# Performance work log

Hardware: AMD Instinct MI355X
Metric: run time of the kernel (lower is better)

## Reference

```python
import jax, jax.numpy as jnp
import numpy as np

B, D, N = 8, 512, 4096
K = 2048  # codebook_size


def setup_inputs() -> dict:
    key = jax.random.key(0)
    k1, k2 = jax.random.split(key)
    x = jax.random.normal(k1, (B, D, N), dtype=jnp.float32)
    embed = jax.random.normal(k2, (K, D), dtype=jnp.float32)
    return {"x": x, "embed": embed}


def reference(x, embed):
    # x: [b, d, n] -> [b, n, d] (project_in is Identity since codebook_dim == dim)
    xt = jnp.transpose(x, (0, 2, 1))  # [b, n, d]
    # squared euclidean distances (argmin-equivalent to torch.cdist argmin)
    x2 = jnp.sum(xt * xt, axis=-1, keepdims=True)          # [b, n, 1]
    e2 = jnp.sum(embed * embed, axis=-1)                   # [k]
    cross = jnp.einsum("bnd,kd->bnk", xt, embed)           # [b, n, k]
    dist = x2 - 2.0 * cross + e2                           # [b, n, k]
    embed_ind = jnp.argmin(dist, axis=-1)                  # [b, n] int
    quantize = embed[embed_ind]                            # [b, n, d] gather
    # project_out Identity, then rearrange 'b n d -> b d n'
    quantize = jnp.transpose(quantize, (0, 2, 1))          # [b, d, n]
    return quantize, embed_ind
```

## Files before the change

### kernel.cpp

```cpp
#include <hip/hip_runtime.h>
#include <math.h>

#define DDIM 512
#define NNN  4096
#define KKK  2048
#define MMM  32768

#define TMQ  128
#define TNC  256
#define BK   32
#define KSPLIT 2
#define KHALF (KKK/KSPLIT)
#define NKT  (KHALF/TNC)
#define NDR  (DDIM/BK)
#define TOTR (NKT*NDR)
#define BUFS ((TMQ+TNC)*BK)
#define NBUF 3
#define TAU  0.05f
#define CAPF 4096

#define XH_OFF   0
#define EH_OFF   8388608
#define PART_OFF (EH_OFF + 524288)
#define XF_OFF   (PART_OFF + MMM*KSPLIT*4)
#define KEY_OFF  (XF_OFF + 2097152)
#define LIST_OFF (KEY_OFF + 8192)
#define CNT_OFF  (LIST_OFF + CAPF)
#define IDX_OFF  ((size_t)MMM * DDIM)

typedef short short8v __attribute__((ext_vector_type(8)));
typedef _Float16 half8v __attribute__((ext_vector_type(8)));
typedef float f32x4   __attribute__((ext_vector_type(4)));

__device__ inline unsigned short f2h(float f) {
  _Float16 h = (_Float16)f;
  return *(unsigned short*)&h;
}

__device__ inline void gl_lds16(const short* g, short* l) {
  __builtin_amdgcn_global_load_lds(
      (const __attribute__((address_space(1))) unsigned int*)g,
      (__attribute__((address_space(3))) unsigned int*)l, 16, 0, 0);
}

__device__ inline unsigned mono(float f) {
  unsigned u = __float_as_uint(f);
  return (u & 0x80000000u) ? ~u : (u | 0x80000000u);
}

__global__ __launch_bounds__(256)
void conv_xe(const float* __restrict__ x, const float* __restrict__ embed,
             float* __restrict__ halfe2, float* __restrict__ out) {
  __shared__ float xt[64][65];
  const int t = threadIdx.x;

  if (blockIdx.x >= 4096) {
    const int blk = blockIdx.x - 4096;
    const int gid = blk * 256 + t;
    if (gid == 0) *(int*)&out[CNT_OFF] = 0;
    if (gid < CAPF) ((unsigned long long*)&out[KEY_OFF])[gid] = ~0ull;
    const int row  = blk * 4 + (t >> 6);
    const int lane = t & 63;
    const float* e = embed + (size_t)row * DDIM;
    short* eh = (short*)&out[EH_OFF];
    const float4 v0 = *(const float4*)&e[lane*8];
    const float4 v1 = *(const float4*)&e[lane*8 + 4];
    const float vv[8] = {v0.x,v0.y,v0.z,v0.w,v1.x,v1.y,v1.z,v1.w};
    float s = 0.f;
    short8v p;
    #pragma unroll
    for (int i = 0; i < 8; ++i) { s = fmaf(vv[i], vv[i], s); p[i] = (short)f2h(vv[i]); }
    *(short8v*)&eh[(size_t)row * DDIM + lane*8] = p;
    #pragma unroll
    for (int off = 32; off >= 1; off >>= 1) s += __shfl_xor(s, off, 64);
    if (lane == 0) halfe2[row] = 0.5f * s;
    return;
  }

  const int nt = blockIdx.x & 63, dt = (blockIdx.x >> 6) & 7, b = blockIdx.x >> 9;
  const int n0 = nt * 64, d0 = dt * 64;
  const float* xb = x + ((size_t)b * DDIM + d0) * NNN + n0;
  #pragma unroll
  for (int i = 0; i < 4; ++i) {
    const int fid = t + 256*i;
    const int dl = fid >> 4, n4 = (fid & 15) * 4;
    const float4 v = *(const float4*)&xb[(size_t)dl * NNN + n4];
    xt[dl][n4+0] = v.x; xt[dl][n4+1] = v.y; xt[dl][n4+2] = v.z; xt[dl][n4+3] = v.w;
  }
  __syncthreads();
  short* xh = (short*)&out[XH_OFF];
  const int m0 = b * NNN + n0;
  #pragma unroll
  for (int i = 0; i < 2; ++i) {
    const int id = t + 256*i;
    const int m = id >> 3, ch = (id & 7) * 8;
    short8v p;
    #pragma unroll
    for (int j = 0; j < 8; ++j) p[j] = (short)f2h(xt[ch + j][m]);
    *(short8v*)&xh[(size_t)(m0 + m) * DDIM + d0 + ch] = p;
  }
}

__global__ __launch_bounds__(256, 2)
void vq_main(const float* __restrict__ halfe2, float* __restrict__ out) {
  __shared__ __align__(16) short lds[NBUF * BUFS];
  const short* xh = (const short*)&out[XH_OFF];
  const short* eh = (const short*)&out[EH_OFF];

  const int t  = threadIdx.x;
  const int mb = blockIdx.x >> 1, ks = blockIdx.x & 1;
  const int q0 = mb * TMQ;
  const int kbase = ks * KHALF;
  const int w = t >> 6, lane = t & 63;
  const int mw = (w >> 1) * 64, nw = (w & 1) * 128;
  const int l15 = lane & 15, lg = lane >> 4;
  const int c0 = w * 6;
  const int lrow = lane >> 2;
  const int scol = ((((lane & 3) - ((lane >> 3) & 3)) & 3) << 3);

  float rv1[16], rv2[16]; int ri1[16];
  #pragma unroll
  for (int i = 0; i < 16; ++i) { rv1[i] = INFINITY; rv2[i] = INFINITY; ri1[i] = 0x7FFFFFFF; }

  auto STAGE = [&](int R, int tb) {
    const int kt_ = R >> 4, dr_ = R & 15;
    const int kb_ = kbase + kt_ * TNC;
    const int d0_ = dr_ * BK;
    short* buf = lds + tb * BUFS;
    #pragma unroll
    for (int j = 0; j < 6; ++j) {
      const int c = c0 + j;
      const short* src = (c < 8)
        ? xh + (size_t)(q0 + c*16 + lrow) * DDIM + d0_ + scol
        : eh + (size_t)(kb_ + (c-8)*16 + lrow) * DDIM + d0_ + scol;
      gl_lds16(src, buf + c * 512);
    }
  };

  STAGE(0, 0);
  STAGE(1, 1);
  asm volatile("s_waitcnt vmcnt(6)" ::: "memory");
  __builtin_amdgcn_s_barrier();

  int bi = 0;
  for (int kt = 0; kt < NKT; ++kt) {
    const int kb = kbase + kt * TNC;
    f32x4 acc[4][8];
    #pragma unroll
    for (int mi = 0; mi < 4; ++mi)
      #pragma unroll
      for (int ni = 0; ni < 8; ++ni) acc[mi][ni] = (f32x4){0.f,0.f,0.f,0.f};

    for (int dr = 0; dr < NDR; ++dr) {
      const int R = kt * NDR + dr;
      const int nb = bi ? bi - 1 : 2;
      if (R + 2 < TOTR) STAGE(R + 2, nb);
      const short* xs = lds + bi * BUFS;
      const short* es = xs + TMQ * BK;
      half8v bfr[8];
      #pragma unroll
      for (int ni = 0; ni < 8; ++ni) {
        const int row = nw + ni*16 + l15;
        bfr[ni] = *(const half8v*)&es[row*32 + (((lg + (row >> 1)) & 3) << 3)];
      }
      #pragma unroll
      for (int mi = 0; mi < 4; ++mi) {
        const int row = mw + mi*16 + l15;
        const half8v a = *(const half8v*)&xs[row*32 + (((lg + (row >> 1)) & 3) << 3)];
        #pragma unroll
        for (int ni = 0; ni < 8; ++ni)
          acc[mi][ni] = __builtin_amdgcn_mfma_f32_16x16x32_f16(a, bfr[ni], acc[mi][ni], 0,0,0);
      }
      if (R + 2 < TOTR) { asm volatile("s_waitcnt vmcnt(6)" ::: "memory"); }
      else              { asm volatile("s_waitcnt vmcnt(0)" ::: "memory"); }
      __builtin_amdgcn_s_barrier();
      bi = (bi == 2) ? 0 : bi + 1;
    }

    float he[8];
    #pragma unroll
    for (int ni = 0; ni < 8; ++ni) he[ni] = halfe2[kb + nw + ni*16 + l15];
    #pragma unroll
    for (int mi = 0; mi < 4; ++mi) {
      #pragma unroll
      for (int r = 0; r < 4; ++r) {
        const int e_ = mi*4 + r;
        #pragma unroll
        for (int ni = 0; ni < 8; ++ni) {
          const float sc = he[ni] - acc[mi][ni][r];
          if (sc < rv1[e_]) { rv2[e_] = rv1[e_]; rv1[e_] = sc; ri1[e_] = kb + nw + ni*16 + l15; }
          else rv2[e_] = fminf(rv2[e_], sc);
        }
      }
    }
  }

  #pragma unroll
  for (int e_ = 0; e_ < 16; ++e_) {
    float v1 = rv1[e_], v2 = rv2[e_]; int i1 = ri1[e_];
    #pragma unroll
    for (int off = 1; off < 16; off <<= 1) {
      const float ov1 = __shfl_xor(v1, off, 64);
      const int   oi1 = __shfl_xor(i1, off, 64);
      const float ov2 = __shfl_xor(v2, off, 64);
      if (ov1 < v1 || (ov1 == v1 && oi1 < i1)) { v2 = fminf(v1, ov2); v1 = ov1; i1 = oi1; }
      else v2 = fminf(v2, ov1);
    }
    rv1[e_] = v1; rv2[e_] = v2; ri1[e_] = i1;
  }

  __syncthreads();
  float* mbuf = (float*)lds;
  if (l15 == 0) {
    #pragma unroll
    for (int mi = 0; mi < 4; ++mi)
      #pragma unroll
      for (int r = 0; r < 4; ++r) {
        const int ql = mw + mi*16 + lg*4 + r;
        const int slot = (ql*2 + (w & 1))*3;
        const int e_ = mi*4 + r;
        mbuf[slot+0] = rv1[e_];
        mbuf[slot+1] = __int_as_float(ri1[e_]);
        mbuf[slot+2] = rv2[e_];
      }
  }
  __syncthreads();
  if (t < TMQ) {
    const float a1 = mbuf[t*6+0]; const int ai = __float_as_int(mbuf[t*6+1]); const float a2 = mbuf[t*6+2];
    const float b1 = mbuf[t*6+3]; const int bi2 = __float_as_int(mbuf[t*6+4]); const float b2 = mbuf[t*6+5];
    float v1, v2; int i1;
    if (b1 < a1 || (b1 == a1 && bi2 < ai)) { v1 = b1; i1 = bi2; v2 = fminf(a1, b2); }
    else                                   { v1 = a1; i1 = ai;  v2 = fminf(a2, b1); }
    f32x4 st = {v1, (float)i1, v2, 0.f};
    *(f32x4*)&out[PART_OFF + ((size_t)(q0 + t)*KSPLIT + ks)*4] = st;
  }
}

__global__ void vq_merge(const float* __restrict__ x, float* __restrict__ out) {
  const int q = blockIdx.x * 256 + threadIdx.x;
  float v1, v2; int i1;
  {
    const f32x4 p = *(const f32x4*)&out[PART_OFF + (size_t)q*(KSPLIT*4)];
    v1 = p[0]; i1 = (int)p[1]; v2 = p[2];
  }
  #pragma unroll
  for (int s = 1; s < KSPLIT; ++s) {
    const f32x4 p = *(const f32x4*)&out[PART_OFF + (size_t)q*(KSPLIT*4) + s*4];
    const float b1 = p[0]; const int bi = (int)p[1]; const float b2 = p[2];
    if (b1 < v1 || (b1 == v1 && bi < i1)) { v2 = fminf(v1, b2); v1 = b1; i1 = bi; }
    else v2 = fminf(v2, b1);
  }
  out[IDX_OFF + q] = (float)i1;
  int pos = -1;
  if (v2 - v1 < TAU) {
    pos = atomicAdd((int*)&out[CNT_OFF], 1);
    if (pos < CAPF) ((int*)&out[LIST_OFF])[pos] = q;
    else pos = -1;
  }
  unsigned long long mask = __ballot(pos >= 0);
  const int lane = threadIdx.x & 63;
  float* XF = &out[XF_OFF];
  while (mask) {
    const int src = __ffsll(mask) - 1;
    mask &= mask - 1;
    const int qq = __shfl(q,   src, 64);
    const int pp = __shfl(pos, src, 64);
    const int bb = qq >> 12, nn = qq & (NNN - 1);
    const float* xb = x + (size_t)bb * DDIM * NNN + nn;
    #pragma unroll
    for (int j = 0; j < 8; ++j) {
      const int d = lane + 64*j;
      XF[(size_t)pp * DDIM + d] = xb[(size_t)d * NNN];
    }
  }
}

__global__ __launch_bounds__(256, 2)
void vq_refine(const float* __restrict__ embed, const float* __restrict__ halfe2,
               float* __restrict__ out) {
  const int nf0 = *(const int*)&out[CNT_OFF];
  const int nf  = nf0 < CAPF ? nf0 : CAPF;
  const int s0  = blockIdx.y * 64;
  if (s0 >= nf) return;
  __shared__ float xs[32][68];
  __shared__ float es[32][132];
  const int t = threadIdx.x, tx = t & 15, ty = t >> 4;
  const int kb = blockIdx.x * 128;
  const float* XF = &out[XF_OFF];
  unsigned long long* keys = (unsigned long long*)&out[KEY_OFF];

  float acc[4][8];
  #pragma unroll
  for (int i = 0; i < 4; ++i)
    #pragma unroll
    for (int j = 0; j < 8; ++j) acc[i][j] = 0.f;

  for (int dc = 0; dc < 16; ++dc) {
    __syncthreads();
    #pragma unroll
    for (int i = 0; i < 2; ++i) {
      const int l = t + 256*i;
      const int m = l >> 3, f = l & 7;
      const float4 v = *(const float4*)&XF[(size_t)(s0 + m) * DDIM + dc*32 + 4*f];
      xs[4*f+0][m] = v.x; xs[4*f+1][m] = v.y; xs[4*f+2][m] = v.z; xs[4*f+3][m] = v.w;
    }
    #pragma unroll
    for (int i = 0; i < 4; ++i) {
      const int l = t + 256*i;
      const int k = l >> 3, f = l & 7;
      const float4 v = *(const float4*)&embed[(size_t)(kb + k)*DDIM + dc*32 + 4*f];
      es[4*f+0][k] = v.x; es[4*f+1][k] = v.y; es[4*f+2][k] = v.z; es[4*f+3][k] = v.w;
    }
    __syncthreads();
    #pragma unroll
    for (int d = 0; d < 32; ++d) {
      const float4 a4 = *(const float4*)&xs[d][ty*4];
      const float4 b0 = *(const float4*)&es[d][tx*4];
      const float4 b1 = *(const float4*)&es[d][64 + tx*4];
      const float a[4]  = {a4.x, a4.y, a4.z, a4.w};
      const float bb[8] = {b0.x, b0.y, b0.z, b0.w, b1.x, b1.y, b1.z, b1.w};
      #pragma unroll
      for (int i = 0; i < 4; ++i)
        #pragma unroll
        for (int j = 0; j < 8; ++j)
          acc[i][j] = fmaf(a[i], bb[j], acc[i][j]);
    }
  }

  const int kb0 = kb + tx*4, kb1 = kb + 64 + tx*4;
  const float4 h0 = *(const float4*)&halfe2[kb0];
  const float4 h1 = *(const float4*)&halfe2[kb1];
  const float hh[8] = {h0.x, h0.y, h0.z, h0.w, h1.x, h1.y, h1.z, h1.w};
  #pragma unroll
  for (int i = 0; i < 4; ++i) {
    float v = hh[0] - acc[i][0];
    int  vi = kb0;
    #pragma unroll
    for (int j = 1; j < 8; ++j) {
      const float w  = hh[j] - acc[i][j];
      const int   wk = (j < 4) ? (kb0 + j) : (kb1 + j - 4);
      if (w < v) { v = w; vi = wk; }
    }
    #pragma unroll
    for (int off = 1; off < 16; off <<= 1) {
      const float ov = __shfl_xor(v, off, 64);
      const int   oi = __shfl_xor(vi, off, 64);
      if (ov < v || (ov == v && oi < vi)) { v = ov; vi = oi; }
    }
    if (tx == 0) {
      const unsigned long long key =
          ((unsigned long long)mono(v) << 32) | (unsigned)vi;
      atomicMin(&keys[s0 + ty*4 + i], key);
    }
  }
}

__global__ void vq_apply(float* __restrict__ out) {
  const int slot = blockIdx.x * 256 + threadIdx.x;
  const int nf0 = *(const int*)&out[CNT_OFF];
  const int nf  = nf0 < CAPF ? nf0 : CAPF;
  if (slot >= nf) return;
  const int q = ((const int*)&out[LIST_OFF])[slot];
  const unsigned long long k = ((const unsigned long long*)&out[KEY_OFF])[slot];
  if (k != ~0ull) out[IDX_OFF + q] = (float)(unsigned)(k & 0xFFFFFFFFull);
}

__global__ __launch_bounds__(256)
void vq_gather(const float* __restrict__ embed, float* __restrict__ out) {
  __shared__ float ls[32][516];
  __shared__ int idx_s[32];
  const int t  = threadIdx.x;
  const int q0 = blockIdx.x * 32;
  const int b  = q0 >> 12, n0 = q0 & (NNN-1);
  if (t < 32) idx_s[t] = (int)out[IDX_OFF + q0 + t];
  __syncthreads();
  {
    const int rh  = t >> 7;
    const int col = (t & 127) * 4;
    #pragma unroll
    for (int p = 0; p < 16; ++p) {
      const int r = p*2 + rh;
      const float4 v = *(const float4*)&embed[(size_t)idx_s[r]*DDIM + col];
      *(float4*)&ls[r][col] = v;
    }
  }
  __syncthreads();
  float* qb = out + (size_t)b * DDIM * NNN + n0;
  #pragma unroll
  for (int j = 0; j < 16; ++j) {
    const int d  = 32*j + (t >> 3);
    const int n4 = (t & 7) * 4;
    float4 v;
    v.x = ls[n4+0][d]; v.y = ls[n4+1][d]; v.z = ls[n4+2][d]; v.w = ls[n4+3][d];
    *(float4*)&qb[(size_t)d * NNN + n4] = v;
  }
}

extern "C" void kernel_launch(void* const* d_in, const int* in_sizes, int n_in,
                              void* d_out, int out_size, void* d_ws, size_t ws_size,
                              hipStream_t stream) {
  const float* x     = (const float*)d_in[0];
  const float* embed = (const float*)d_in[1];
  float* out    = (float*)d_out;
  float* halfe2 = (float*)d_ws;

  hipLaunchKernelGGL(conv_xe, dim3(4096 + KKK/4), dim3(256), 0, stream, x, embed, halfe2, out);
  hipLaunchKernelGGL(vq_main,  dim3((MMM/TMQ)*KSPLIT), dim3(256), 0, stream, halfe2, out);
  hipLaunchKernelGGL(vq_merge, dim3(MMM/256), dim3(256), 0, stream, x, out);
  hipLaunchKernelGGL(vq_refine,dim3(16, CAPF/64), dim3(256), 0, stream, embed, halfe2, out);
  hipLaunchKernelGGL(vq_apply, dim3(CAPF/256),dim3(256), 0, stream, out);
  hipLaunchKernelGGL(vq_gather,dim3(MMM/32),  dim3(256), 0, stream, embed, out);
}
```

Baseline: 267.1 us.

## Fuse split-K merge into main and apply into refine via last-block tickets

Removes two kernel launches by having the last-arriving block of each split pair merge partial argmin results inside vq_main, and the last refine block apply refined indices. It also shrinks the LDS pipeline from triple to double buffering with a full vmcnt(0) wait each step. This cuts launch overhead and intermediate global round trips. The price is atomic tickets and a shallower prefetch pipeline that may expose more load latency in the main GEMM loop.

```diff
diff --git a/kernel.cpp b/kernel.cpp
--- a/kernel.cpp
+++ b/kernel.cpp
@@ -15,7 +15,7 @@
 #define NDR  (DDIM/BK)
 #define TOTR (NKT*NDR)
 #define BUFS ((TMQ+TNC)*BK)
-#define NBUF 3
+#define NBUF 2
 #define TAU  0.05f
 #define CAPF 4096
 
@@ -26,6 +26,7 @@
 #define KEY_OFF  (XF_OFF + 2097152)
 #define LIST_OFF (KEY_OFF + 8192)
 #define CNT_OFF  (LIST_OFF + CAPF)
+#define TICK_OFF (CNT_OFF + 1)
 #define IDX_OFF  ((size_t)MMM * DDIM)
 
 typedef short short8v __attribute__((ext_vector_type(8)));
@@ -58,6 +59,7 @@
     const int blk = blockIdx.x - 4096;
     const int gid = blk * 256 + t;
     if (gid == 0) *(int*)&out[CNT_OFF] = 0;
+    if (gid < 257) ((int*)&out[TICK_OFF])[gid] = 0;
     if (gid < CAPF) ((unsigned long long*)&out[KEY_OFF])[gid] = ~0ull;
     const int row  = blk * 4 + (t >> 6);
     const int lane = t & 63;
@@ -102,7 +104,8 @@
 }
 
 __global__ __launch_bounds__(256, 2)
-void vq_main(const float* __restrict__ halfe2, float* __restrict__ out) {
+void vq_main(const float* __restrict__ x, const float* __restrict__ halfe2,
+             float* __restrict__ out) {
   __shared__ __align__(16) short lds[NBUF * BUFS];
   const short* xh = (const short*)&out[XH_OFF];
   const short* eh = (const short*)&out[EH_OFF];
@@ -122,11 +125,11 @@
   #pragma unroll
   for (int i = 0; i < 16; ++i) { rv1[i] = INFINITY; rv2[i] = INFINITY; ri1[i] = 0x7FFFFFFF; }
 
-  auto STAGE = [&](int R, int tb) {
+  auto STAGE = [&](int R) {
     const int kt_ = R >> 4, dr_ = R & 15;
     const int kb_ = kbase + kt_ * TNC;
     const int d0_ = dr_ * BK;
-    short* buf = lds + tb * BUFS;
+    short* buf = lds + (R & 1) * BUFS;
     #pragma unroll
     for (int j = 0; j < 6; ++j) {
       const int c = c0 + j;
@@ -137,12 +140,10 @@
     }
   };
 
-  STAGE(0, 0);
-  STAGE(1, 1);
-  asm volatile("s_waitcnt vmcnt(6)" ::: "memory");
+  STAGE(0);
+  asm volatile("s_waitcnt vmcnt(0)" ::: "memory");
   __builtin_amdgcn_s_barrier();
 
-  int bi = 0;
   for (int kt = 0; kt < NKT; ++kt) {
     const int kb = kbase + kt * TNC;
     f32x4 acc[4][8];
@@ -151,12 +152,13 @@
       #pragma unroll
       for (int ni = 0; ni < 8; ++ni) acc[mi][ni] = (f32x4){0.f,0.f,0.f,0.f};
 
+    #pragma unroll 2
     for (int dr = 0; dr < NDR; ++dr) {
       const int R = kt * NDR + dr;
-      const int nb = bi ? bi - 1 : 2;
-      if (R + 2 < TOTR) STAGE(R + 2, nb);
-      const short* xs = lds + bi * BUFS;
-      const short* es = xs + TMQ * BK;
+      const short* cur = lds + (R & 1) * BUFS;
+      if (R + 1 < TOTR) STAGE(R + 1);
+      const short* xs = cur;
+      const short* es = cur + TMQ * BK;
       half8v bfr[8];
       #pragma unroll
       for (int ni = 0; ni < 8; ++ni) {
@@ -171,10 +173,8 @@
         for (int ni = 0; ni < 8; ++ni)
           acc[mi][ni] = __builtin_amdgcn_mfma_f32_16x16x32_f16(a, bfr[ni], acc[mi][ni], 0,0,0);
       }
-      if (R + 2 < TOTR) { asm volatile("s_waitcnt vmcnt(6)" ::: "memory"); }
-      else              { asm volatile("s_waitcnt vmcnt(0)" ::: "memory"); }
+      asm volatile("s_waitcnt vmcnt(0)" ::: "memory");
       __builtin_amdgcn_s_barrier();
-      bi = (bi == 2) ? 0 : bi + 1;
     }
 
     float he[8];
@@ -225,40 +225,52 @@
       }
   }
   __syncthreads();
+  unsigned long long* PART = (unsigned long long*)&out[PART_OFF];
   if (t < TMQ) {
     const float a1 = mbuf[t*6+0]; const int ai = __float_as_int(mbuf[t*6+1]); const float a2 = mbuf[t*6+2];
     const float b1 = mbuf[t*6+3]; const int bi2 = __float_as_int(mbuf[t*6+4]); const float b2 = mbuf[t*6+5];
     float v1, v2; int i1;
     if (b1 < a1 || (b1 == a1 && bi2 < ai)) { v1 = b1; i1 = bi2; v2 = fminf(a1, b2); }
     else                                   { v1 = a1; i1 = ai;  v2 = fminf(a2, b1); }
-    f32x4 st = {v1, (float)i1, v2, 0.f};
-    *(f32x4*)&out[PART_OFF + ((size_t)(q0 + t)*KSPLIT + ks)*4] = st;
-  }
-}
-
-__global__ void vq_merge(const float* __restrict__ x, float* __restrict__ out) {
-  const int q = blockIdx.x * 256 + threadIdx.x;
-  float v1, v2; int i1;
-  {
-    const f32x4 p = *(const f32x4*)&out[PART_OFF + (size_t)q*(KSPLIT*4)];
-    v1 = p[0]; i1 = (int)p[1]; v2 = p[2];
-  }
-  #pragma unroll
-  for (int s = 1; s < KSPLIT; ++s) {
-    const f32x4 p = *(const f32x4*)&out[PART_OFF + (size_t)q*(KSPLIT*4) + s*4];
-    const float b1 = p[0]; const int bi = (int)p[1]; const float b2 = p[2];
-    if (b1 < v1 || (b1 == v1 && bi < i1)) { v2 = fminf(v1, b2); v1 = b1; i1 = bi; }
-    else v2 = fminf(v2, b1);
-  }
-  out[IDX_OFF + q] = (float)i1;
+    const unsigned long long pa =
+        ((unsigned long long)__float_as_uint(v1) << 32) | (unsigned)i1;
+    const unsigned long long pb = (unsigned long long)__float_as_uint(v2);
+    __hip_atomic_store(&PART[(size_t)(q0 + t)*4 + ks*2 + 0], pa,
+                       __ATOMIC_RELEASE, __HIP_MEMORY_SCOPE_AGENT);
+    __hip_atomic_store(&PART[(size_t)(q0 + t)*4 + ks*2 + 1], pb,
+                       __ATOMIC_RELEASE, __HIP_MEMORY_SCOPE_AGENT);
+  }
+  __syncthreads();
+  __shared__ int who;
+  int* tick = (int*)&out[TICK_OFF];
+  if (t == 0)
+    who = __hip_atomic_fetch_add(&tick[mb], 1, __ATOMIC_ACQ_REL, __HIP_MEMORY_SCOPE_AGENT);
+  __syncthreads();
+  if (who != 1) return;
+
   int pos = -1;
-  if (v2 - v1 < TAU) {
-    pos = atomicAdd((int*)&out[CNT_OFF], 1);
-    if (pos < CAPF) ((int*)&out[LIST_OFF])[pos] = q;
-    else pos = -1;
+  const int q = q0 + (t & 127);
+  if (t < TMQ) {
+    const unsigned long long a0 = __hip_atomic_load(&PART[(size_t)q*4 + 0], __ATOMIC_ACQUIRE, __HIP_MEMORY_SCOPE_AGENT);
+    const unsigned long long a1 = __hip_atomic_load(&PART[(size_t)q*4 + 1], __ATOMIC_ACQUIRE, __HIP_MEMORY_SCOPE_AGENT);
+    const unsigned long long b0 = __hip_atomic_load(&PART[(size_t)q*4 + 2], __ATOMIC_ACQUIRE, __HIP_MEMORY_SCOPE_AGENT);
+    const unsigned long long b1 = __hip_atomic_load(&PART[(size_t)q*4 + 3], __ATOMIC_ACQUIRE, __HIP_MEMORY_SCOPE_AGENT);
+    float v1 = __uint_as_float((unsigned)(a0 >> 32));
+    int   i1 = (int)(unsigned)a0;
+    float v2 = __uint_as_float((unsigned)a1);
+    const float w1 = __uint_as_float((unsigned)(b0 >> 32));
+    const int   wi = (int)(unsigned)b0;
+    const float w2 = __uint_as_float((unsigned)b1);
+    if (w1 < v1 || (w1 == v1 && wi < i1)) { v2 = fminf(v1, w2); v1 = w1; i1 = wi; }
+    else v2 = fminf(v2, w1);
+    out[IDX_OFF + q] = (float)i1;
+    if (v2 - v1 < TAU) {
+      pos = atomicAdd((int*)&out[CNT_OFF], 1);
+      if (pos < CAPF) ((int*)&out[LIST_OFF])[pos] = q;
+      else pos = -1;
+    }
   }
   unsigned long long mask = __ballot(pos >= 0);
-  const int lane = threadIdx.x & 63;
   float* XF = &out[XF_OFF];
   while (mask) {
     const int src = __ffsll(mask) - 1;
@@ -281,7 +293,6 @@
   const int nf0 = *(const int*)&out[CNT_OFF];
   const int nf  = nf0 < CAPF ? nf0 : CAPF;
   const int s0  = blockIdx.y * 64;
-  if (s0 >= nf) return;
   __shared__ float xs[32][68];
   __shared__ float es[32][132];
   const int t = threadIdx.x, tx = t & 15, ty = t >> 4;
@@ -289,80 +300,87 @@
   const float* XF = &out[XF_OFF];
   unsigned long long* keys = (unsigned long long*)&out[KEY_OFF];
 
-  float acc[4][8];
-  #pragma unroll
-  for (int i = 0; i < 4; ++i)
-    #pragma unroll
-    for (int j = 0; j < 8; ++j) acc[i][j] = 0.f;
-
-  for (int dc = 0; dc < 16; ++dc) {
-    __syncthreads();
-    #pragma unroll
-    for (int i = 0; i < 2; ++i) {
-      const int l = t + 256*i;
-      const int m = l >> 3, f = l & 7;
-      const float4 v = *(const float4*)&XF[(size_t)(s0 + m) * DDIM + dc*32 + 4*f];
-      xs[4*f+0][m] = v.x; xs[4*f+1][m] = v.y; xs[4*f+2][m] = v.z; xs[4*f+3][m] = v.w;
-    }
+  if (s0 < nf) {
+    float acc[4][8];
+    #pragma unroll
+    for (int i = 0; i < 4; ++i)
+      #pragma unroll
+      for (int j = 0; j < 8; ++j) acc[i][j] = 0.f;
+
+    for (int dc = 0; dc < 16; ++dc) {
+      __syncthreads();
+      #pragma unroll
+      for (int i = 0; i < 2; ++i) {
+        const int l = t + 256*i;
+        const int m = l >> 3, f = l & 7;
+        const float4 v = *(const float4*)&XF[(size_t)(s0 + m) * DDIM + dc*32 + 4*f];
+        xs[4*f+0][m] = v.x; xs[4*f+1][m] = v.y; xs[4*f+2][m] = v.z; xs[4*f+3][m] = v.w;
+      }
+      #pragma unroll
+      for (int i = 0; i < 4; ++i) {
+        const int l = t + 256*i;
+        const int k = l >> 3, f = l & 7;
+        const float4 v = *(const float4*)&embed[(size_t)(kb + k)*DDIM + dc*32 + 4*f];
+        es[4*f+0][k] = v.x; es[4*f+1][k] = v.y; es[4*f+2][k] = v.z; es[4*f+3][k] = v.w;
+      }
+      __syncthreads();
+      #pragma unroll
+      for (int d = 0; d < 32; ++d) {
+        const float4 a4 = *(const float4*)&xs[d][ty*4];
+        const float4 b0 = *(const float4*)&es[d][tx*4];
+        const float4 b1 = *(const float4*)&es[d][64 + tx*4];
+        const float a[4]  = {a4.x, a4.y, a4.z, a4.w};
+        const float bb[8] = {b0.x, b0.y, b0.z, b0.w, b1.x, b1.y, b1.z, b1.w};
+        #pragma unroll
+        for (int i = 0; i < 4; ++i)
+          #pragma unroll
+          for (int j = 0; j < 8; ++j)
+            acc[i][j] = fmaf(a[i], bb[j], acc[i][j]);
+      }
+    }
+
+    const int kb0 = kb + tx*4, kb1 = kb + 64 + tx*4;
+    const float4 h0 = *(const float4*)&halfe2[kb0];
+    const float4 h1 = *(const float4*)&halfe2[kb1];
+    const float hh[8] = {h0.x, h0.y, h0.z, h0.w, h1.x, h1.y, h1.z, h1.w};
     #pragma unroll
     for (int i = 0; i < 4; ++i) {
-      const int l = t + 256*i;
-      const int k = l >> 3, f = l & 7;
-      const float4 v = *(const float4*)&embed[(size_t)(kb + k)*DDIM + dc*32 + 4*f];
-      es[4*f+0][k] = v.x; es[4*f+1][k] = v.y; es[4*f+2][k] = v.z; es[4*f+3][k] = v.w;
-    }
-    __syncthreads();
-    #pragma unroll
-    for (int d = 0; d < 32; ++d) {
-      const float4 a4 = *(const float4*)&xs[d][ty*4];
-      const float4 b0 = *(const float4*)&es[d][tx*4];
-      const float4 b1 = *(const float4*)&es[d][64 + tx*4];
-      const float a[4]  = {a4.x, a4.y, a4.z, a4.w};
-      const float bb[8] = {b0.x, b0.y, b0.z, b0.w, b1.x, b1.y, b1.z, b1.w};
-      #pragma unroll
-      for (int i = 0; i < 4; ++i)
-        #pragma unroll
-        for (int j = 0; j < 8; ++j)
-          acc[i][j] = fmaf(a[i], bb[j], acc[i][j]);
-    }
-  }
-
-  const int kb0 = kb + tx*4, kb1 = kb + 64 + tx*4;
-  const float4 h0 = *(const float4*)&halfe2[kb0];
-  const float4 h1 = *(const float4*)&halfe2[kb1];
-  const float hh[8] = {h0.x, h0.y, h0.z, h0.w, h1.x, h1.y, h1.z, h1.w};
-  #pragma unroll
-  for (int i = 0; i < 4; ++i) {
-    float v = hh[0] - acc[i][0];
-    int  vi = kb0;
-    #pragma unroll
-    for (int j = 1; j < 8; ++j) {
-      const float w  = hh[j] - acc[i][j];
-      const int   wk = (j < 4) ? (kb0 + j) : (kb1 + j - 4);
-      if (w < v) { v = w; vi = wk; }
-    }
-    #pragma unroll
-    for (int off = 1; off < 16; off <<= 1) {
-      const float ov = __shfl_xor(v, off, 64);
-      const int   oi = __shfl_xor(vi, off, 64);
-      if (ov < v || (ov == v && oi < vi)) { v = ov; vi = oi; }
-    }
-    if (tx == 0) {
-      const unsigned long long key =
-          ((unsigned long long)mono(v) << 32) | (unsigned)vi;
-      atomicMin(&keys[s0 + ty*4 + i], key);
-    }
-  }
-}
-
-__global__ void vq_apply(float* __restrict__ out) {
-  const int slot = blockIdx.x * 256 + threadIdx.x;
-  const int nf0 = *(const int*)&out[CNT_OFF];
-  const int nf  = nf0 < CAPF ? nf0 : CAPF;
-  if (slot >= nf) return;
-  const int q = ((const int*)&out[LIST_OFF])[slot];
-  const unsigned long long k = ((const unsigned long long*)&out[KEY_OFF])[slot];
-  if (k != ~0ull) out[IDX_OFF + q] = (float)(unsigned)(k & 0xFFFFFFFFull);
+      float v = hh[0] - acc[i][0];
+      int  vi = kb0;
+      #pragma unroll
+      for (int j = 1; j < 8; ++j) {
+        const float w  = hh[j] - acc[i][j];
+        const int   wk = (j < 4) ? (kb0 + j) : (kb1 + j - 4);
+        if (w < v) { v = w; vi = wk; }
+      }
+      #pragma unroll
+      for (int off = 1; off < 16; off <<= 1) {
+        const float ov = __shfl_xor(v, off, 64);
+        const int   oi = __shfl_xor(vi, off, 64);
+        if (ov < v || (ov == v && oi < vi)) { v = ov; vi = oi; }
+      }
+      if (tx == 0) {
+        const unsigned long long key =
+            ((unsigned long long)mono(v) << 32) | (unsigned)vi;
+        atomicMin(&keys[s0 + ty*4 + i], key);
+      }
+    }
+  }
+
+  __syncthreads();
+  __shared__ int rwho;
+  if (t == 0)
+    rwho = __hip_atomic_fetch_add(&((int*)&out[TICK_OFF])[256], 1,
+                                  __ATOMIC_ACQ_REL, __HIP_MEMORY_SCOPE_AGENT);
+  __syncthreads();
+  if (rwho != 16*(CAPF/64) - 1) return;
+  const int* list = (const int*)&out[LIST_OFF];
+  for (int slot = t; slot < nf; slot += 256) {
+    const unsigned long long k =
+        __hip_atomic_load((const unsigned long long*)&out[KEY_OFF] + slot,
+                          __ATOMIC_ACQUIRE, __HIP_MEMORY_SCOPE_AGENT);
+    if (k != ~0ull) out[IDX_OFF + list[slot]] = (float)(unsigned)(k & 0xFFFFFFFFull);
+  }
 }
 
 __global__ __launch_bounds__(256)
@@ -405,9 +423,7 @@
   float* halfe2 = (float*)d_ws;
 
   hipLaunchKernelGGL(conv_xe, dim3(4096 + KKK/4), dim3(256), 0, stream, x, embed, halfe2, out);
-  hipLaunchKernelGGL(vq_main,  dim3((MMM/TMQ)*KSPLIT), dim3(256), 0, stream, halfe2, out);
-  hipLaunchKernelGGL(vq_merge, dim3(MMM/256), dim3(256), 0, stream, x, out);
+  hipLaunchKernelGGL(vq_main,  dim3((MMM/TMQ)*KSPLIT), dim3(256), 0, stream, x, halfe2, out);
   hipLaunchKernelGGL(vq_refine,dim3(16, CAPF/64), dim3(256), 0, stream, embed, halfe2, out);
-  hipLaunchKernelGGL(vq_apply, dim3(CAPF/256),dim3(256), 0, stream, out);
   hipLaunchKernelGGL(vq_gather,dim3(MMM/32),  dim3(256), 0, stream, embed, out);
 }
```

Result: slower. 319.9 us (+19.8%).
